# Optimization experiments

Hardware: AMD Instinct MI355X
Metric: run time of the kernel (lower is better)

Reference implementation:

```python
import jax, jax.numpy as jnp
import numpy as np

N = 128          # preconditioner matrix dim = 8*8*2
L8 = 8           # lattice extent
KAPPA = 0.276
MAXITER = 20
NENT = N * (N + 1) // 2  # 8256 lower-triangular entries
_rows, _cols = np.tril_indices(N)

G = [jnp.array([[0, 1], [1, 0]], dtype=jnp.complex64),          # gamma_1 = sigma_x
     jnp.array([[0, -1j], [1j, 0]], dtype=jnp.complex64)]        # gamma_2 = sigma_y
I2 = jnp.eye(2, dtype=jnp.complex64)


def _D(x, U):
    # Wilson-Dirac: x (B,8,8,2) spinor field, U (B,2,8,8) complex links.
    out = x
    for mu in range(2):
        ax = mu + 1
        Um = U[:, mu]                                  # U_mu(n)
        Umb = jnp.roll(jnp.conj(Um), 1, axis=ax)       # U_mu^dag(n-mu)
        fwd = Um[..., None] * jnp.roll(x, -1, axis=ax)  # U(n) x(n+mu)
        bwd = Umb[..., None] * jnp.roll(x, 1, axis=ax)  # U^dag(n-mu) x(n-mu)
        out = out - KAPPA * (jnp.einsum('st,bxyt->bxys', I2 - G[mu], fwd)
                             + jnp.einsum('st,bxyt->bxys', I2 + G[mu], bwd))
    return out


def _Ddag(y, U):
    # Adjoint of _D: projectors swap on forward/backward hops.
    out = y
    for mu in range(2):
        ax = mu + 1
        Um = U[:, mu]
        Umb = jnp.roll(jnp.conj(Um), 1, axis=ax)
        fwd = Um[..., None] * jnp.roll(y, -1, axis=ax)
        bwd = Umb[..., None] * jnp.roll(y, 1, axis=ax)
        out = out - KAPPA * (jnp.einsum('st,bxyt->bxys', I2 + G[mu], fwd)
                             + jnp.einsum('st,bxyt->bxys', I2 - G[mu], bwd))
    return out


def setup_inputs() -> dict:
    key = jax.random.key(0)
    k1, k2, k3, k4 = jax.random.split(key, 4)
    B = 2048
    return {
        'net_out_re': jax.random.normal(k1, (B, NENT), jnp.float32),
        'net_out_im': jax.random.normal(k2, (B, NENT), jnp.float32),
        'theta': jax.random.normal(k3, (B, 2, L8, L8), jnp.float32),
        'b': jax.random.uniform(k4, (B, L8, L8, 2), jnp.float32),
    }


def reference(net_out_re, net_out_im, theta, b):
    net_out = (net_out_re + 1j * net_out_im).astype(jnp.complex64)  # (B, 8256)
    U = jnp.exp(1j * theta).astype(jnp.complex64)                   # (B, 2, 8, 8)
    bc = b.astype(jnp.complex64)                                    # (B, 8, 8, 2)
    B = bc.shape[0]

    # Dense lower-triangular factor (scatter of net_out, as in upper_tri_mat).
    Lmat = jnp.zeros((B, N, N), jnp.complex64).at[:, _rows, _cols].set(net_out)

    def M(x):  # preconditioner: L^H (L v)
        v = x.reshape(B, -1)
        w = jnp.einsum('bij,bj->bi', Lmat, v)
        u = jnp.einsum('bji,bj->bi', jnp.conj(Lmat), w)
        return u.reshape(x.shape)

    def A(x):  # DDOpt = D^dag D (Hermitian PSD)
        return _Ddag(_D(x, U), U)

    def dot(a, c):  # batched complex inner product
        return jnp.sum(jnp.conj(a) * c, axis=(1, 2, 3), keepdims=True)

    x0 = jnp.zeros_like(bc)
    r = bc - A(x0)
    z = M(r)
    p = z
    rz = dot(r, z)

    def step(carry, _):
        x, r, p, rz = carry
        Ap = A(p)
        alpha = rz / dot(p, Ap)
        x = x + alpha * p
        r = r - alpha * Ap
        z = M(r)
        rz2 = dot(r, z)
        p = z + (rz2 / rz) * p
        return (x, r, p, rz2), None

    (x, _, _, _), _ = jax.lax.scan(step, (x0, r, p, rz), None, length=MAXITER)

    res = A(x) - bc
    rn = jnp.linalg.norm(res.reshape(B, -1), axis=1)  # real per-batch norms
    return jnp.mean(rn).astype(jnp.float32)
```

## Files before the change

### kernel.cpp

```cpp
#include <hip/hip_runtime.h>
#include <math.h>

#define NV 128
#define NTRI 8256
#define NPAD 8320
#define KAP 0.276f
#define MAXIT 20
#define TPB 512

__device__ __forceinline__ float2 f2(float x, float y){ return make_float2(x, y); }
__device__ __forceinline__ float2 cadd(float2 a, float2 b){ return make_float2(a.x+b.x, a.y+b.y); }
__device__ __forceinline__ float2 csub(float2 a, float2 b){ return make_float2(a.x-b.x, a.y-b.y); }
__device__ __forceinline__ float2 cmul(float2 a, float2 b){ return make_float2(a.x*b.x - a.y*b.y, a.x*b.y + a.y*b.x); }
__device__ __forceinline__ float2 cmulc(float2 a, float2 b){
  return make_float2(a.x*b.x + a.y*b.y, a.x*b.y - a.y*b.x); }
__device__ __forceinline__ float2 cmac(float2 acc, float2 a, float2 b){
  acc.x = fmaf(a.x, b.x, fmaf(-a.y, b.y, acc.x));
  acc.y = fmaf(a.x, b.y, fmaf( a.y, b.x, acc.y));
  return acc; }
__device__ __forceinline__ float2 cmacc(float2 acc, float2 a, float2 b){
  acc.x = fmaf(a.x, b.x, fmaf( a.y, b.y, acc.x));
  acc.y = fmaf(a.x, b.y, fmaf(-a.y, b.x, acc.y));
  return acc; }
__device__ __forceinline__ float2 cdiv(float2 n, float2 d){
  float s = 1.0f / fmaf(d.x, d.x, d.y*d.y);
  return make_float2((n.x*d.x + n.y*d.y)*s, (n.y*d.x - n.x*d.y)*s); }

__device__ __forceinline__ int rowoff(int r){ return ((r*(r+1)) >> 1) + ((r+1) >> 1); }

template<int EF>
__device__ __forceinline__ void dirac(const float2* __restrict__ U,
                                      const float2* __restrict__ vin,
                                      float2* __restrict__ vout, int t)
{
  if (t < NV) {
    const int s = t & 1, site = t >> 1;
    const int yi = site & 7, xi = site >> 3;
    const int xp = (xi+1)&7, xm = (xi-1)&7, yp = (yi+1)&7, ym = (yi-1)&7;
    float2 acc;
    {
      const int bf = (xp<<4) + (yi<<1);
      float2 fs = vin[bf + s], fo = vin[bf + (s^1)];
      float2 cf = (EF > 0) ? cadd(fs, fo) : csub(fs, fo);
      acc = cmul(U[(xi<<3)+yi], cf);
      const int bb = (xm<<4) + (yi<<1);
      float2 bs = vin[bb + s], bo = vin[bb + (s^1)];
      float2 cb = (EF > 0) ? csub(bs, bo) : cadd(bs, bo);
      acc = cadd(acc, cmulc(U[(xm<<3)+yi], cb));
    }
    {
      const float tg = s ? 1.0f : -1.0f;
      const float gf = (float)EF * tg;
      const int bf = (xi<<4) + (yp<<1);
      float2 fs = vin[bf + s], fo = vin[bf + (s^1)];
      float2 cf = make_float2(fmaf(-gf, fo.y, fs.x), fmaf(gf, fo.x, fs.y));
      acc = cadd(acc, cmul(U[64 + (xi<<3)+yi], cf));
      const float gb = -gf;
      const int bb = (xi<<4) + (ym<<1);
      float2 bs = vin[bb + s], bo = vin[bb + (s^1)];
      float2 cb = make_float2(fmaf(-gb, bo.y, bs.x), fmaf(gb, bo.x, bs.y));
      acc = cadd(acc, cmulc(U[64 + (xi<<3)+ym], cb));
    }
    float2 v0 = vin[t];
    vout[t] = make_float2(fmaf(-KAP, acc.x, v0.x), fmaf(-KAP, acc.y, v0.y));
  }
  __syncthreads();
}

__device__ __forceinline__ void precond(const float2* __restrict__ Lc2,
                                        const float2* __restrict__ vin,
                                        float2* __restrict__ wvv,
                                        float2* __restrict__ vout,
                                        int w, int g, int c)
{
  {
    const int r = (w << 4) + g;
    const int bR = rowoff(r);
    float2 acc = f2(0.f, 0.f);
    const int kc = w << 1;
    for (int k = 0; k < kc; ++k) {
      const int j0 = (k << 3) + (c << 1);
      float4 Lp = *(const float4*)&Lc2[bR + j0];
      float4 vp = *(const float4*)&vin[j0];
      acc = cmac(acc, f2(Lp.x, Lp.y), f2(vp.x, vp.y));
      acc = cmac(acc, f2(Lp.z, Lp.w), f2(vp.z, vp.w));
    }
    #pragma unroll
    for (int pk = 0; pk < 2; ++pk) {
      const int j0 = ((kc + pk) << 3) + (c << 1);
      float4 Lp = *(const float4*)&Lc2[bR + j0];
      float4 vp = *(const float4*)&vin[j0];
      float2 La = (j0     <= r) ? f2(Lp.x, Lp.y) : f2(0.f, 0.f);
      float2 Lb = (j0 + 1 <= r) ? f2(Lp.z, Lp.w) : f2(0.f, 0.f);
      acc = cmac(acc, La, f2(vp.x, vp.y));
      acc = cmac(acc, Lb, f2(vp.z, vp.w));
    }
    acc.x += __shfl_xor(acc.x, 1); acc.y += __shfl_xor(acc.y, 1);
    acc.x += __shfl_xor(acc.x, 2); acc.y += __shfl_xor(acc.y, 2);
    if (c == 0) wvv[r] = acc;
  }
  __syncthreads();
  {
    const int j = (w << 4) + g;
    float2 acc = f2(0.f, 0.f);
    const int kc = (w << 1) + 2;
    #pragma unroll
    for (int pk = 0; pk < 2; ++pk) {
      const int i0 = ((2*w + pk) << 3) + (c << 1);
      float2 La = Lc2[rowoff(i0)     + j];
      float2 Lb = Lc2[rowoff(i0 + 1) + j];
      float4 wp = *(const float4*)&wvv[i0];
      if (i0     < j) La = f2(0.f, 0.f);
      if (i0 + 1 < j) Lb = f2(0.f, 0.f);
      acc = cmacc(acc, La, f2(wp.x, wp.y));
      acc = cmacc(acc, Lb, f2(wp.z, wp.w));
    }
    for (int k = kc; k < 16; ++k) {
      const int i0 = (k << 3) + (c << 1);
      float2 La = Lc2[rowoff(i0)     + j];
      float2 Lb = Lc2[rowoff(i0 + 1) + j];
      float4 wp = *(const float4*)&wvv[i0];
      acc = cmacc(acc, La, f2(wp.x, wp.y));
      acc = cmacc(acc, Lb, f2(wp.z, wp.w));
    }
    acc.x += __shfl_xor(acc.x, 1); acc.y += __shfl_xor(acc.y, 1);
    acc.x += __shfl_xor(acc.x, 2); acc.y += __shfl_xor(acc.y, 2);
    if (c == 0) vout[j] = acc;
  }
  __syncthreads();
}

__device__ __forceinline__ float2 block_dot(const float2* __restrict__ a, const float2* __restrict__ c,
                            float2* __restrict__ scal, int t, int slot)
{
  if (t < NV) {
    float2 v = cmacc(f2(0.f,0.f), a[t], c[t]);
    #pragma unroll
    for (int off = 32; off > 0; off >>= 1) {
      v.x += __shfl_down(v.x, off, 64);
      v.y += __shfl_down(v.y, off, 64);
    }
    if ((t & 63) == 0) scal[(slot<<1) + (t >> 6)] = v;
  }
  __syncthreads();
  return cadd(scal[slot<<1], scal[(slot<<1)+1]);
}

extern "C" __global__ void __launch_bounds__(TPB, 4)
cg_loss_kernel(const float* __restrict__ nre, const float* __restrict__ nim,
               const float* __restrict__ theta, const float* __restrict__ bin,
               float* __restrict__ out, float invB)
{
  __shared__ __align__(16) float2 Lc2[NPAD];
  __shared__ __align__(16) float2 Uc[128];
  __shared__ __align__(16) float2 bv[NV], xv[NV], rv[NV], pv[NV];
  __shared__ __align__(16) float2 zv[NV], Apv[NV], tv[NV], wv[NV];
  __shared__ float2 scal[8];

  const int t = threadIdx.x;
  const long long b = blockIdx.x;
  const int w = t >> 6, lane = t & 63, g = lane >> 2, c = lane & 3;

  {
    const float* nreb = nre + b * NTRI;
    const float* nimb = nim + b * NTRI;
    for (int p = t; p < NTRI; p += TPB) {
      float re = nreb[p], im = nimb[p];
      int r = (int)((sqrtf(8.f * (float)p + 1.f) - 1.f) * 0.5f + 1e-3f);
      int tr = (r * (r + 1)) >> 1;
      if (tr > p)               { tr -= r; --r; }
      else if (tr + r + 1 <= p) { tr += r + 1; ++r; }
      const int jj = p - tr;
      Lc2[tr + ((r + 1) >> 1) + jj] = make_float2(re, im);
    }
  }
  if (t < NV) {
    float th = theta[b * 128 + t];
    float sn, cs;
    sincosf(th, &sn, &cs);
    Uc[t] = make_float2(cs, sn);
    float bb = bin[b * 128 + t];
    bv[t] = make_float2(bb, 0.f);
    xv[t] = make_float2(0.f, 0.f);
    rv[t] = make_float2(bb, 0.f);
  }
  __syncthreads();

  precond(Lc2, rv, wv, zv, w, g, c);
  if (t < NV) pv[t] = zv[t];
  float2 rz = block_dot(rv, zv, scal, t, 0);

  #pragma unroll 1
  for (int it = 0; it < MAXIT; ++it) {
    dirac<-1>(Uc, pv, tv, t);
    dirac<+1>(Uc, tv, Apv, t);
    float2 pAp = block_dot(pv, Apv, scal, t, 1);
    if (t < NV) {
      float2 alpha = cdiv(rz, pAp);
      xv[t] = cmac(xv[t], alpha, pv[t]);
      rv[t] = csub(rv[t], cmul(alpha, Apv[t]));
    }
    __syncthreads();
    precond(Lc2, rv, wv, zv, w, g, c);
    float2 rz2 = block_dot(rv, zv, scal, t, 0);
    if (t < NV) {
      float2 beta = cdiv(rz2, rz);
      pv[t] = cmac(zv[t], beta, pv[t]);
    }
    rz = rz2;
    __syncthreads();
  }

  dirac<-1>(Uc, xv, tv, t);
  dirac<+1>(Uc, tv, Apv, t);
  if (t < NV) {
    float2 d = csub(Apv[t], bv[t]);
    float v = fmaf(d.x, d.x, d.y * d.y);
    #pragma unroll
    for (int off = 32; off > 0; off >>= 1) v += __shfl_down(v, off, 64);
    if ((t & 63) == 0) scal[4 + (t >> 6)].x = v;
  }
  __syncthreads();
  if (t == 0) {
    float rn = sqrtf(scal[4].x + scal[5].x);
    atomicAdd(out, rn * invB);
  }
}

extern "C" void kernel_launch(void* const* d_in, const int* in_sizes, int n_in,
                              void* d_out, int out_size, void* d_ws, size_t ws_size,
                              hipStream_t stream)
{
  const float* nre   = (const float*)d_in[0];
  const float* nim   = (const float*)d_in[1];
  const float* theta = (const float*)d_in[2];
  const float* bin   = (const float*)d_in[3];
  float* out = (float*)d_out;
  const int B = in_sizes[0] / NTRI;

  hipMemsetAsync(out, 0, sizeof(float), stream);
  cg_loss_kernel<<<B, TPB, 0, stream>>>(nre, nim, theta, bin, out, 1.0f / (float)B);
}
```

Before: 514.3 us.

## Reorganize L into 16-row blocked layout, cache L^H columns in registers, balance rows

```diff
diff --git a/kernel.cpp b/kernel.cpp
--- a/kernel.cpp
+++ b/kernel.cpp
@@ -3,7 +3,7 @@
 
 #define NV 128
 #define NTRI 8256
-#define NPAD 8320
+#define NB 9216
 #define KAP 0.276f
 #define MAXIT 20
 #define TPB 512
@@ -26,7 +26,10 @@
   float s = 1.0f / fmaf(d.x, d.x, d.y*d.y);
   return make_float2((n.x*d.x + n.y*d.y)*s, (n.y*d.x - n.x*d.y)*s); }
 
-__device__ __forceinline__ int rowoff(int r){ return ((r*(r+1)) >> 1) + ((r+1) >> 1); }
+__device__ __forceinline__ int offB(int i, int j){
+  const int m = i >> 4;
+  return 128*m*(m+1) + ((i & 15) << 4)*(m+1) + j;
+}
 
 template<int EF>
 __device__ __forceinline__ void dirac(const float2* __restrict__ U,
@@ -67,65 +70,66 @@
   __syncthreads();
 }
 
+__device__ __forceinline__ float2 oct_reduce(float2 v){
+  v.x += __shfl_xor(v.x, 1); v.y += __shfl_xor(v.y, 1);
+  v.x += __shfl_xor(v.x, 2); v.y += __shfl_xor(v.y, 2);
+  v.x += __shfl_xor(v.x, 4); v.y += __shfl_xor(v.y, 4);
+  return v;
+}
+
 __device__ __forceinline__ void precond(const float2* __restrict__ Lc2,
+                                        const float2 LL[8][2], const float2 LS[4][2],
                                         const float2* __restrict__ vin,
-                                        float2* __restrict__ wvv,
+                                        float2* __restrict__ twv,
                                         float2* __restrict__ vout,
-                                        int w, int g, int c)
-{
-  {
-    const int r = (w << 4) + g;
-    const int bR = rowoff(r);
-    float2 acc = f2(0.f, 0.f);
-    const int kc = w << 1;
-    for (int k = 0; k < kc; ++k) {
-      const int j0 = (k << 3) + (c << 1);
-      float4 Lp = *(const float4*)&Lc2[bR + j0];
+                                        int w, int oct, int cp)
+{
+  const int rS = (w << 3) + oct, rL = 127 - rS;
+  const int jL = rS, jS = rL;
+  {
+    const int tS = ((w << 3) + 23) >> 4;
+    const int tL = (143 - (w << 3)) >> 4;
+    const int mS = rS >> 4, mL = rL >> 4;
+    const int baseS = 128*mS*(mS+1) + ((rS & 15) << 4)*(mS+1);
+    const int baseL = 128*mL*(mL+1) + ((rL & 15) << 4)*(mL+1);
+    float2 aS = f2(0.f,0.f), aL = f2(0.f,0.f);
+    for (int k = 0; k < tS; ++k) {
+      const int j0 = (k << 4) + (cp << 1);
+      float4 Lp = *(const float4*)&Lc2[baseS + j0];
       float4 vp = *(const float4*)&vin[j0];
-      acc = cmac(acc, f2(Lp.x, Lp.y), f2(vp.x, vp.y));
-      acc = cmac(acc, f2(Lp.z, Lp.w), f2(vp.z, vp.w));
-    }
+      aS = cmac(aS, f2(Lp.x, Lp.y), f2(vp.x, vp.y));
+      aS = cmac(aS, f2(Lp.z, Lp.w), f2(vp.z, vp.w));
+    }
+    for (int k = 0; k < tL; ++k) {
+      const int j0 = (k << 4) + (cp << 1);
+      float4 Lp = *(const float4*)&Lc2[baseL + j0];
+      float4 vp = *(const float4*)&vin[j0];
+      aL = cmac(aL, f2(Lp.x, Lp.y), f2(vp.x, vp.y));
+      aL = cmac(aL, f2(Lp.z, Lp.w), f2(vp.z, vp.w));
+    }
+    aS = oct_reduce(aS);
+    aL = oct_reduce(aL);
+    if (cp == 0) twv[rS] = aS;
+    if (cp == 1) twv[rL] = aL;
+  }
+  __syncthreads();
+  {
+    float2 aL2 = f2(0.f,0.f), aS2 = f2(0.f,0.f);
     #pragma unroll
-    for (int pk = 0; pk < 2; ++pk) {
-      const int j0 = ((kc + pk) << 3) + (c << 1);
-      float4 Lp = *(const float4*)&Lc2[bR + j0];
-      float4 vp = *(const float4*)&vin[j0];
-      float2 La = (j0     <= r) ? f2(Lp.x, Lp.y) : f2(0.f, 0.f);
-      float2 Lb = (j0 + 1 <= r) ? f2(Lp.z, Lp.w) : f2(0.f, 0.f);
-      acc = cmac(acc, La, f2(vp.x, vp.y));
-      acc = cmac(acc, Lb, f2(vp.z, vp.w));
-    }
-    acc.x += __shfl_xor(acc.x, 1); acc.y += __shfl_xor(acc.y, 1);
-    acc.x += __shfl_xor(acc.x, 2); acc.y += __shfl_xor(acc.y, 2);
-    if (c == 0) wvv[r] = acc;
-  }
-  __syncthreads();
-  {
-    const int j = (w << 4) + g;
-    float2 acc = f2(0.f, 0.f);
-    const int kc = (w << 1) + 2;
-    #pragma unroll
-    for (int pk = 0; pk < 2; ++pk) {
-      const int i0 = ((2*w + pk) << 3) + (c << 1);
-      float2 La = Lc2[rowoff(i0)     + j];
-      float2 Lb = Lc2[rowoff(i0 + 1) + j];
-      float4 wp = *(const float4*)&wvv[i0];
-      if (i0     < j) La = f2(0.f, 0.f);
-      if (i0 + 1 < j) Lb = f2(0.f, 0.f);
-      acc = cmacc(acc, La, f2(wp.x, wp.y));
-      acc = cmacc(acc, Lb, f2(wp.z, wp.w));
-    }
-    for (int k = kc; k < 16; ++k) {
-      const int i0 = (k << 3) + (c << 1);
-      float2 La = Lc2[rowoff(i0)     + j];
-      float2 Lb = Lc2[rowoff(i0 + 1) + j];
-      float4 wp = *(const float4*)&wvv[i0];
-      acc = cmacc(acc, La, f2(wp.x, wp.y));
-      acc = cmacc(acc, Lb, f2(wp.z, wp.w));
-    }
-    acc.x += __shfl_xor(acc.x, 1); acc.y += __shfl_xor(acc.y, 1);
-    acc.x += __shfl_xor(acc.x, 2); acc.y += __shfl_xor(acc.y, 2);
-    if (c == 0) vout[j] = acc;
+    for (int k = 0; k < 8; ++k) {
+      float4 wp = *(const float4*)&twv[(k << 4) + (cp << 1)];
+      float2 w0 = f2(wp.x, wp.y), w1 = f2(wp.z, wp.w);
+      aL2 = cmacc(aL2, LL[k][0], w0);
+      aL2 = cmacc(aL2, LL[k][1], w1);
+      if (k >= 4) {
+        aS2 = cmacc(aS2, LS[k-4][0], w0);
+        aS2 = cmacc(aS2, LS[k-4][1], w1);
+      }
+    }
+    aL2 = oct_reduce(aL2);
+    aS2 = oct_reduce(aS2);
+    if (cp == 0) vout[jL] = aL2;
+    if (cp == 1) vout[jS] = aS2;
   }
   __syncthreads();
 }
@@ -151,16 +155,20 @@
                const float* __restrict__ theta, const float* __restrict__ bin,
                float* __restrict__ out, float invB)
 {
-  __shared__ __align__(16) float2 Lc2[NPAD];
+  __shared__ __align__(16) float2 Lc2[NB];
   __shared__ __align__(16) float2 Uc[128];
-  __shared__ __align__(16) float2 bv[NV], xv[NV], rv[NV], pv[NV];
-  __shared__ __align__(16) float2 zv[NV], Apv[NV], tv[NV], wv[NV];
+  __shared__ __align__(16) float2 rv[NV], pv[NV], zv[NV], Apv[NV], twv[NV];
   __shared__ float2 scal[8];
 
   const int t = threadIdx.x;
   const long long b = blockIdx.x;
-  const int w = t >> 6, lane = t & 63, g = lane >> 2, c = lane & 3;
-
+  const int w = t >> 6, lane = t & 63, oct = lane >> 3, cp = lane & 7;
+
+  {
+    float4* L4 = (float4*)Lc2;
+    for (int i = t; i < NB/2; i += TPB) L4[i] = make_float4(0.f,0.f,0.f,0.f);
+  }
+  __syncthreads();
   {
     const float* nreb = nre + b * NTRI;
     const float* nimb = nim + b * NTRI;
@@ -170,38 +178,54 @@
       int tr = (r * (r + 1)) >> 1;
       if (tr > p)               { tr -= r; --r; }
       else if (tr + r + 1 <= p) { tr += r + 1; ++r; }
-      const int jj = p - tr;
-      Lc2[tr + ((r + 1) >> 1) + jj] = make_float2(re, im);
-    }
-  }
+      Lc2[offB(r, p - tr)] = make_float2(re, im);
+    }
+  }
+  float2 xr = f2(0.f, 0.f);
   if (t < NV) {
     float th = theta[b * 128 + t];
     float sn, cs;
     sincosf(th, &sn, &cs);
     Uc[t] = make_float2(cs, sn);
     float bb = bin[b * 128 + t];
-    bv[t] = make_float2(bb, 0.f);
-    xv[t] = make_float2(0.f, 0.f);
     rv[t] = make_float2(bb, 0.f);
   }
   __syncthreads();
 
-  precond(Lc2, rv, wv, zv, w, g, c);
+  const int jL = (w << 3) + oct, jS = 127 - jL;
+  float2 LL[8][2], LS[4][2];
+  #pragma unroll
+  for (int k = 0; k < 8; ++k) {
+    const int i0 = (k << 4) + (cp << 1), i1 = i0 + 1;
+    const int base = (128*k + 32*cp) * (k + 1);
+    float2 a = Lc2[base + jL];
+    float2 c = Lc2[base + ((k + 1) << 4) + jL];
+    LL[k][0] = (i0 >= jL) ? a : f2(0.f,0.f);
+    LL[k][1] = (i1 >= jL) ? c : f2(0.f,0.f);
+    if (k >= 4) {
+      float2 d = Lc2[base + jS];
+      float2 e = Lc2[base + ((k + 1) << 4) + jS];
+      LS[k-4][0] = (i0 >= jS) ? d : f2(0.f,0.f);
+      LS[k-4][1] = (i1 >= jS) ? e : f2(0.f,0.f);
+    }
+  }
+
+  precond(Lc2, LL, LS, rv, twv, zv, w, oct, cp);
   if (t < NV) pv[t] = zv[t];
   float2 rz = block_dot(rv, zv, scal, t, 0);
 
   #pragma unroll 1
   for (int it = 0; it < MAXIT; ++it) {
-    dirac<-1>(Uc, pv, tv, t);
-    dirac<+1>(Uc, tv, Apv, t);
+    dirac<-1>(Uc, pv, twv, t);
+    dirac<+1>(Uc, twv, Apv, t);
     float2 pAp = block_dot(pv, Apv, scal, t, 1);
     if (t < NV) {
       float2 alpha = cdiv(rz, pAp);
-      xv[t] = cmac(xv[t], alpha, pv[t]);
+      xr = cmac(xr, alpha, pv[t]);
       rv[t] = csub(rv[t], cmul(alpha, Apv[t]));
     }
     __syncthreads();
-    precond(Lc2, rv, wv, zv, w, g, c);
+    precond(Lc2, LL, LS, rv, twv, zv, w, oct, cp);
     float2 rz2 = block_dot(rv, zv, scal, t, 0);
     if (t < NV) {
       float2 beta = cdiv(rz2, rz);
@@ -211,10 +235,13 @@
     __syncthreads();
   }
 
-  dirac<-1>(Uc, xv, tv, t);
-  dirac<+1>(Uc, tv, Apv, t);
-  if (t < NV) {
-    float2 d = csub(Apv[t], bv[t]);
+  if (t < NV) zv[t] = xr;
+  __syncthreads();
+  dirac<-1>(Uc, zv, twv, t);
+  dirac<+1>(Uc, twv, Apv, t);
+  if (t < NV) {
+    float bb = bin[b * 128 + t];
+    float2 d = csub(Apv[t], f2(bb, 0.f));
     float v = fmaf(d.x, d.x, d.y * d.y);
     #pragma unroll
     for (int off = 32; off > 0; off >>= 1) v += __shfl_down(v, off, 64);
```

New measurement: 792.2 us. 54.0% more time.
